# Kernel optimization log

Measured on AMD Instinct MI355X. Metric: run time of the kernel, lower is better.

Reference implementation:

```python
import jax, jax.numpy as jnp
import numpy as np

B, T, D = 16, 8192, 512
NHEAD, NKV = 8, 2
HD = D // NHEAD            # 64
KV_DIM = NKV * HD          # 128
N_REP = NHEAD // NKV       # 4
SCALE = 1.0 / np.sqrt(HD)


def setup_inputs() -> dict:
    key = jax.random.key(0)
    ks = jax.random.split(key, 8)
    w = 0.02
    return {
        "query": jax.random.normal(ks[0], (B, D), dtype=jnp.float32),
        "enc": jax.random.normal(ks[1], (B, T, D), dtype=jnp.float32),
        "Wq": jax.random.normal(ks[2], (D, D), dtype=jnp.float32) * w,
        "Wk": jax.random.normal(ks[3], (D, KV_DIM), dtype=jnp.float32) * w,
        "Wv": jax.random.normal(ks[4], (D, KV_DIM), dtype=jnp.float32) * w,
        "W1": jax.random.normal(ks[5], (2 * D, 4 * D), dtype=jnp.float32) * w,
        "W2": jax.random.normal(ks[6], (4 * D, D), dtype=jnp.float32) * w,
    }


def reference(query, enc, Wq, Wk, Wv, W1, W2):
    # Q projection: single decoder step -> [B, H, HD]
    q = (query @ Wq).reshape(B, NHEAD, HD)
    # K/V projections (GQA): [B, T, NKV, HD] -> [B, NKV, T, HD]
    k = (enc @ Wk).reshape(B, T, NKV, HD).transpose(0, 2, 1, 3)
    v = (enc @ Wv).reshape(B, T, NKV, HD).transpose(0, 2, 1, 3)
    # repeat KV heads to match query heads: [B, H, T, HD]
    k = jnp.repeat(k, N_REP, axis=1)
    v = jnp.repeat(v, N_REP, axis=1)
    # scaled dot-product attention, Tq == 1
    scores = jnp.einsum("bhd,bhtd->bht", q, k) * SCALE        # [B, H, T]
    attn = jax.nn.softmax(scores, axis=-1)
    context = jnp.einsum("bht,bhtd->bhd", attn, v).reshape(B, D)
    # combine context with query through SwiGLU-style MLP (Linear-SiLU-Linear)
    h = jnp.concatenate([context, query], axis=-1)            # [B, 2D]
    out = jax.nn.silu(h @ W1) @ W2                            # [B, D]
    return out
```

## Files before the change

### kernel.cpp

```cpp
#include <hip/hip_runtime.h>
#include <hip/hip_bf16.h>
#include <cstdint>
#include <cstddef>

#define BB 16
#define TT 8192
#define DD 512
#define NHEAD 8
#define NKV 2
#define HD 64
#define KVD 128
#define SCALE 0.125f

#define RB 64
#define NCHUNK (TT / RB)
#define BK 32
#define NSTEP (DD / BK)

typedef __attribute__((ext_vector_type(8))) short bf16x8;
typedef __attribute__((ext_vector_type(4))) float f32x4;

#define WS_Q      0
#define WS_WBT    8192
#define WS_OPART  73728
#define WS_ML     1122304
#define WS_H      1155072
#define WS_APART  1171456
#define WS_M2     1728512

__device__ __forceinline__ ushort f2bf(float f) {
    uint u = __builtin_bit_cast(uint, f);
    u += 0x7fffu + ((u >> 16) & 1u);
    return (ushort)(u >> 16);
}
__device__ __forceinline__ uint cvtpk(float a, float b) {
    uint r;
    asm("v_cvt_pk_bf16_f32 %0, %1, %2" : "=v"(r) : "v"(a), "v"(b));
    return r;
}
__device__ __forceinline__ float bf1(ushort s) {
    return __builtin_bit_cast(float, (uint)s << 16);
}
__device__ __forceinline__ float bflo(uint u) {
    return __builtin_bit_cast(float, u << 16);
}
__device__ __forceinline__ float bfhi(uint u) {
    return __builtin_bit_cast(float, u & 0xffff0000u);
}

__global__ __launch_bounds__(256) void k_prep(const float* __restrict__ Wk,
                                              const float* __restrict__ Wv,
                                              const float* __restrict__ query,
                                              const float* __restrict__ Wq,
                                              ushort* __restrict__ wbt4,
                                              float* __restrict__ wsq) {
    const int t = threadIdx.x;
    if (blockIdx.x < 64) {
        const int G0 = blockIdx.x * 2048 + t * 8;
        const int s = G0 >> 13, r = G0 & 8191;
        const int fid = r >> 9, lane = (r >> 3) & 63;
        const int col = (fid >> 2) * 64 + (fid & 3) * 16 + (lane & 15);
        const int kbase = s * 32 + (lane >> 4) * 8;
        const float* W = (col < KVD) ? (Wk + col) : (Wv + (col - KVD));
#pragma unroll
        for (int e = 0; e < 8; ++e)
            wbt4[G0 + e] = f2bf(W[(size_t)(kbase + e) * KVD]);
    } else {
        __shared__ float qrow[DD];
        const int x = blockIdx.x - 64;
        const int b = x >> 1, half = x & 1;
        qrow[t] = query[b * DD + t];
        qrow[t + 256] = query[b * DD + t + 256];
        __syncthreads();
        const int col = half * 256 + t;
        float a0 = 0.f;
#pragma unroll 8
        for (int d = 0; d < DD; ++d) a0 = fmaf(qrow[d], Wq[(size_t)d * DD + col], a0);
        wsq[b * DD + col] = a0;
    }
}

__global__ __launch_bounds__(256) void k_attn(const float* __restrict__ enc,
                                              const ushort* __restrict__ wbt4,
                                              const float* __restrict__ wsq,
                                              float* __restrict__ o_part,
                                              float* __restrict__ ml) {
    __shared__ __align__(16) char smem[33024];
    __shared__ float sc[NHEAD * RB];
    __shared__ float qs[DD];

    const int tid = threadIdx.x;
    const int chunk = blockIdx.x, b = blockIdx.y;
    const int lane = tid & 63, w = tid >> 6;

    qs[tid] = wsq[b * DD + tid] * SCALE;
    qs[tid + 256] = wsq[b * DD + tid + 256] * SCALE;

    char* const A0 = smem;
    char* const A1 = smem + 4096;
    ushort* const kvl = (ushort*)smem;

    const float* encb = enc + ((size_t)b * TT + (size_t)chunk * RB) * DD;
    const ushort* wfr = wbt4 + ((size_t)w * 256 + lane) * 8;

    const int srow = (tid >> 6) * 16 + (tid & 15);
    const int skb = ((tid >> 4) & 3) * 8;

    f32x4 acc[4][4];
#pragma unroll
    for (int i = 0; i < 4; ++i)
#pragma unroll
        for (int j = 0; j < 4; ++j) acc[i][j] = (f32x4){0.f, 0.f, 0.f, 0.f};

    float4 eA0, eA1, eB0, eB1;
    bf16x8 bfA[4], bfB[4], af[4];

#define LOAD_E(E0, E1, ss)                                                           \
    {                                                                                \
        const float* p_ = encb + (size_t)srow * DD + (ss) * BK + skb;                \
        E0 = *(const float4*)p_;                                                     \
        E1 = *(const float4*)(p_ + 4);                                               \
    }
#define WRITE_A(Abuf, E0, E1)                                                        \
    {                                                                                \
        uint4 u_;                                                                    \
        u_.x = cvtpk(E0.x, E0.y);                                                    \
        u_.y = cvtpk(E0.z, E0.w);                                                    \
        u_.z = cvtpk(E1.x, E1.y);                                                    \
        u_.w = cvtpk(E1.z, E1.w);                                                    \
        *(uint4*)((Abuf) + tid * 16) = u_;                                           \
    }
#define LOAD_B(BF, ss)                                                               \
    {                                                                                \
        _Pragma("unroll") for (int nt = 0; nt < 4; ++nt)                             \
            BF[nt] = *(const bf16x8*)(wfr + (size_t)(ss) * 8192 + nt * 512);         \
    }
#define SYNC()                                                                       \
    {                                                                                \
        __builtin_amdgcn_sched_barrier(0);                                           \
        asm volatile("s_waitcnt lgkmcnt(0)" ::: "memory");                           \
        __builtin_amdgcn_s_barrier();                                                \
    }
#define MFMA_STEP(Ac, BF)                                                            \
    {                                                                                \
        _Pragma("unroll") for (int rt = 0; rt < 4; ++rt)                             \
            af[rt] = *(const bf16x8*)((Ac) + (rt * 64 + lane) * 16);                 \
        _Pragma("unroll") for (int rt = 0; rt < 4; ++rt)                             \
            _Pragma("unroll") for (int nt = 0; nt < 4; ++nt)                         \
                acc[rt][nt] = __builtin_amdgcn_mfma_f32_16x16x32_bf16(               \
                    af[rt], BF[nt], acc[rt][nt], 0, 0, 0);                           \
    }

    LOAD_E(eA0, eA1, 0);
    LOAD_B(bfA, 0);
    LOAD_E(eB0, eB1, 1);
    WRITE_A(A0, eA0, eA1);
    LOAD_E(eA0, eA1, 2);
    SYNC();

#pragma unroll
    for (int s = 0; s < NSTEP; ++s) {
        char* const Ac = (s & 1) ? A1 : A0;
        char* const An = (s & 1) ? A0 : A1;
        if ((s & 1) == 0) {
            if (s + 1 < NSTEP) WRITE_A(An, eB0, eB1);
            if (s + 3 < NSTEP) LOAD_E(eB0, eB1, s + 3);
            if (s + 1 < NSTEP) LOAD_B(bfB, s + 1);
            MFMA_STEP(Ac, bfA);
        } else {
            if (s + 1 < NSTEP) WRITE_A(An, eA0, eA1);
            if (s + 3 < NSTEP) LOAD_E(eA0, eA1, s + 3);
            if (s + 1 < NSTEP) LOAD_B(bfA, s + 1);
            MFMA_STEP(Ac, bfB);
        }
        SYNC();
    }

    const int h0 = w * 2;
    const int kvh = h0 >> 2;

    __syncthreads();
#pragma unroll
    for (int rt = 0; rt < 4; ++rt)
#pragma unroll
        for (int nt = 0; nt < 4; ++nt) {
            const int col = w * 64 + nt * 16 + (lane & 15);
#pragma unroll
            for (int j = 0; j < 4; ++j) {
                const int row = rt * 16 + (lane >> 4) * 4 + j;
                kvl[row * 258 + col] = f2bf(acc[rt][nt][j]);
            }
        }
    __syncthreads();

    {
        const float* qh0 = qs + h0 * HD;
        const float* qh1 = qs + (h0 + 1) * HD;
        const uint* kr = (const uint*)(kvl + lane * 258 + kvh * HD);
        float s0 = 0.f, s1 = 0.f;
#pragma unroll
        for (int d2 = 0; d2 < 32; ++d2) {
            const uint u = kr[d2];
            const float klo = bflo(u), khi = bfhi(u);
            s0 = fmaf(klo, qh0[2 * d2], s0);
            s0 = fmaf(khi, qh0[2 * d2 + 1], s0);
            s1 = fmaf(klo, qh1[2 * d2], s1);
            s1 = fmaf(khi, qh1[2 * d2 + 1], s1);
        }
        sc[h0 * RB + lane] = s0;
        sc[(h0 + 1) * RB + lane] = s1;
    }
    __syncthreads();

    {
        float mx0 = -1e30f, mx1 = -1e30f;
#pragma unroll 8
        for (int r = 0; r < RB; ++r) {
            mx0 = fmaxf(mx0, sc[h0 * RB + r]);
            mx1 = fmaxf(mx1, sc[(h0 + 1) * RB + r]);
        }
        float l0 = 0.f, l1 = 0.f, o0 = 0.f, o1 = 0.f;
        const ushort* vcol = kvl + KVD + kvh * HD + lane;
#pragma unroll 4
        for (int r = 0; r < RB; ++r) {
            const float vv = bf1(vcol[r * 258]);
            const float p0 = __expf(sc[h0 * RB + r] - mx0);
            const float p1 = __expf(sc[(h0 + 1) * RB + r] - mx1);
            l0 += p0; o0 = fmaf(p0, vv, o0);
            l1 += p1; o1 = fmaf(p1, vv, o1);
        }
        const size_t base0 = ((size_t)b * NCHUNK + chunk) * NHEAD + h0;
        o_part[base0 * HD + lane] = o0;
        o_part[(base0 + 1) * HD + lane] = o1;
        if (lane == 0) {
            ml[base0 * 2] = mx0; ml[base0 * 2 + 1] = l0;
            ml[(base0 + 1) * 2] = mx1; ml[(base0 + 1) * 2 + 1] = l1;
        }
    }
#undef LOAD_E
#undef WRITE_A
#undef LOAD_B
#undef SYNC
#undef MFMA_STEP
}

__global__ __launch_bounds__(512) void k_reduce(const float* __restrict__ o_part,
                                                const float* __restrict__ ml,
                                                const float* __restrict__ query,
                                                float* __restrict__ hvec) {
    __shared__ float sEl[NHEAD][NCHUNK];
    const int b = blockIdx.x, t = threadIdx.x;
    const int h = t >> 6, lane = t & 63;

    const size_t ma_i = (((size_t)b * NCHUNK + lane) * NHEAD + h) * 2;
    const size_t mb_i = (((size_t)b * NCHUNK + lane + 64) * NHEAD + h) * 2;
    const float ma = ml[ma_i], la = ml[ma_i + 1];
    const float mb = ml[mb_i], lb = ml[mb_i + 1];
    float M = fmaxf(ma, mb);
#pragma unroll
    for (int off = 32; off >= 1; off >>= 1) M = fmaxf(M, __shfl_xor(M, off));
    const float ea = __expf(ma - M), eb = __expf(mb - M);
    float L = la * ea + lb * eb;
#pragma unroll
    for (int off = 32; off >= 1; off >>= 1) L += __shfl_xor(L, off);
    sEl[h][lane] = ea;
    sEl[h][lane + 64] = eb;
    __syncthreads();

    float O = 0.f;
#pragma unroll 4
    for (int i = 0; i < NCHUNK; ++i) {
        const size_t base = ((size_t)b * NCHUNK + i) * NHEAD + h;
        O = fmaf(o_part[base * HD + lane], sEl[h][i], O);
    }
    hvec[b * 1024 + h * HD + lane] = O / L;
    hvec[b * 1024 + 512 + t] = query[b * DD + t];
}

__global__ __launch_bounds__(256) void k_mlp1(const float* __restrict__ hvec,
                                              const float* __restrict__ W1,
                                              float* __restrict__ apart) {
    const int jb = blockIdx.x, ib = blockIdx.y;
    const int j = jb * 256 + threadIdx.x;
    float acc[BB];
#pragma unroll
    for (int b = 0; b < BB; ++b) acc[b] = 0.f;
    for (int i0 = ib * 64; i0 < ib * 64 + 64; i0 += 4) {
        const float w0 = W1[(size_t)(i0 + 0) * 2048 + j];
        const float w1 = W1[(size_t)(i0 + 1) * 2048 + j];
        const float w2 = W1[(size_t)(i0 + 2) * 2048 + j];
        const float w3 = W1[(size_t)(i0 + 3) * 2048 + j];
#pragma unroll
        for (int b = 0; b < BB; ++b) {
            const float* hb = hvec + b * 1024 + i0;
            acc[b] = fmaf(hb[0], w0, acc[b]);
            acc[b] = fmaf(hb[1], w1, acc[b]);
            acc[b] = fmaf(hb[2], w2, acc[b]);
            acc[b] = fmaf(hb[3], w3, acc[b]);
        }
    }
#pragma unroll
    for (int b = 0; b < BB; ++b)
        apart[((size_t)ib * BB + b) * 2048 + j] = acc[b];
}

__global__ __launch_bounds__(256) void k_mlp2(const float* __restrict__ apart,
                                              const float* __restrict__ W2,
                                              float* __restrict__ m2part) {
    __shared__ float actl[256];
    const int jb = blockIdx.x, b = blockIdx.y, ib = blockIdx.z;
    const int t = threadIdx.x;
    {
        const int jglob = ib * 256 + t;
        float s = 0.f;
#pragma unroll
        for (int p = 0; p < 16; ++p) s += apart[((size_t)p * BB + b) * 2048 + jglob];
        actl[t] = s / (1.f + __expf(-s));
    }
    __syncthreads();
    const int d = jb * 256 + t;
    float acc = 0.f;
    for (int j0 = 0; j0 < 256; j0 += 4) {
        const int jg = ib * 256 + j0;
        acc = fmaf(actl[j0 + 0], W2[(size_t)(jg + 0) * 512 + d], acc);
        acc = fmaf(actl[j0 + 1], W2[(size_t)(jg + 1) * 512 + d], acc);
        acc = fmaf(actl[j0 + 2], W2[(size_t)(jg + 2) * 512 + d], acc);
        acc = fmaf(actl[j0 + 3], W2[(size_t)(jg + 3) * 512 + d], acc);
    }
    m2part[((size_t)ib * BB + b) * 512 + d] = acc;
}

__global__ __launch_bounds__(512) void k_out(const float* __restrict__ m2part,
                                             float* __restrict__ out) {
    const int b = blockIdx.x, t = threadIdx.x;
    float s = 0.f;
#pragma unroll
    for (int ib = 0; ib < 8; ++ib) s += m2part[((size_t)ib * BB + b) * 512 + t];
    out[b * DD + t] = s;
}

extern "C" void kernel_launch(void* const* d_in, const int* in_sizes, int n_in,
                              void* d_out, int out_size, void* d_ws, size_t ws_size,
                              hipStream_t stream) {
    const float* query = (const float*)d_in[0];
    const float* enc   = (const float*)d_in[1];
    const float* Wq    = (const float*)d_in[2];
    const float* Wk    = (const float*)d_in[3];
    const float* Wv    = (const float*)d_in[4];
    const float* W1    = (const float*)d_in[5];
    const float* W2    = (const float*)d_in[6];
    float* ws  = (float*)d_ws;
    float* out = (float*)d_out;
    ushort* wbt4 = (ushort*)(ws + WS_WBT);

    k_prep<<<dim3(96), dim3(256), 0, stream>>>(Wk, Wv, query, Wq, wbt4, ws + WS_Q);
    k_attn<<<dim3(NCHUNK, BB), dim3(256), 0, stream>>>(enc, wbt4, ws + WS_Q,
                                                       ws + WS_OPART, ws + WS_ML);
    k_reduce<<<dim3(BB), dim3(512), 0, stream>>>(ws + WS_OPART, ws + WS_ML, query, ws + WS_H);
    k_mlp1<<<dim3(8, 16), dim3(256), 0, stream>>>(ws + WS_H, W1, ws + WS_APART);
    k_mlp2<<<dim3(2, BB, 8), dim3(256), 0, stream>>>(ws + WS_APART, W2, ws + WS_M2);
    k_out<<<dim3(BB), dim3(512), 0, stream>>>(ws + WS_M2, out);
}
```

Measured before the change: 147.7 us.

## Process two K-steps per barrier in attention GEMM and fuse MLP2 with output reduction

The attention projection loop now handles two BK slices per sync period, using four LDS A buffers and wider enc prefetches. This halves the number of barriers and gives more loads in flight per wait. Separately, k_mlp2 now reduces over all 2048 hidden units inside one block, using four k-slices and an LDS reduction, and writes the output directly. That removes the k_out launch and the partial-sum buffer, but each block recomputes the SiLU activations for all 2048 units.

```diff
diff --git a/kernel.cpp b/kernel.cpp
--- a/kernel.cpp
+++ b/kernel.cpp
@@ -16,6 +16,7 @@
 #define NCHUNK (TT / RB)
 #define BK 32
 #define NSTEP (DD / BK)
+#define NPER (NSTEP / 2)
 
 typedef __attribute__((ext_vector_type(8))) short bf16x8;
 typedef __attribute__((ext_vector_type(4))) float f32x4;
@@ -26,7 +27,6 @@
 #define WS_ML     1122304
 #define WS_H      1155072
 #define WS_APART  1171456
-#define WS_M2     1728512
 
 __device__ __forceinline__ ushort f2bf(float f) {
     uint u = __builtin_bit_cast(uint, f);
@@ -98,6 +98,8 @@
 
     char* const A0 = smem;
     char* const A1 = smem + 4096;
+    char* const A2 = smem + 8192;
+    char* const A3 = smem + 12288;
     ushort* const kvl = (ushort*)smem;
 
     const float* encb = enc + ((size_t)b * TT + (size_t)chunk * RB) * DD;
@@ -112,14 +114,16 @@
 #pragma unroll
         for (int j = 0; j < 4; ++j) acc[i][j] = (f32x4){0.f, 0.f, 0.f, 0.f};
 
-    float4 eA0, eA1, eB0, eB1;
+    float4 e00, e01, e02, e03, e10, e11, e12, e13;
     bf16x8 bfA[4], bfB[4], af[4];
 
-#define LOAD_E(E0, E1, ss)                                                           \
-    {                                                                                \
-        const float* p_ = encb + (size_t)srow * DD + (ss) * BK + skb;                \
-        E0 = *(const float4*)p_;                                                     \
-        E1 = *(const float4*)(p_ + 4);                                               \
+#define LOAD_E2(Ea, Eb, Ec, Ed, s0)                                                  \
+    {                                                                                \
+        const float* p_ = encb + (size_t)srow * DD + (s0) * BK + skb;                \
+        Ea = *(const float4*)p_;                                                     \
+        Eb = *(const float4*)(p_ + 4);                                               \
+        Ec = *(const float4*)(p_ + BK);                                              \
+        Ed = *(const float4*)(p_ + BK + 4);                                          \
     }
 #define WRITE_A(Abuf, E0, E1)                                                        \
     {                                                                                \
@@ -150,31 +154,37 @@
                 acc[rt][nt] = __builtin_amdgcn_mfma_f32_16x16x32_bf16(               \
                     af[rt], BF[nt], acc[rt][nt], 0, 0, 0);                           \
     }
-
-    LOAD_E(eA0, eA1, 0);
+#define DO_PERIOD(p, EW0, EW1, EW2, EW3)                                             \
+    {                                                                                \
+        char* const Ac0_ = ((p) & 1) ? A2 : A0;                                      \
+        char* const Ac1_ = ((p) & 1) ? A3 : A1;                                      \
+        char* const An0_ = ((p) & 1) ? A0 : A2;                                      \
+        char* const An1_ = ((p) & 1) ? A1 : A3;                                      \
+        if ((p) + 1 < NPER) { WRITE_A(An0_, EW0, EW1); WRITE_A(An1_, EW2, EW3); }    \
+        if ((p) < NPER - 3) LOAD_E2(EW0, EW1, EW2, EW3, 2 * (p) + 6);                \
+        LOAD_B(bfB, 2 * (p) + 1);                                                    \
+        MFMA_STEP(Ac0_, bfA);                                                        \
+        if ((p) + 1 < NPER) LOAD_B(bfA, 2 * (p) + 2);                                \
+        MFMA_STEP(Ac1_, bfB);                                                        \
+        SYNC();                                                                      \
+    }
+
+    LOAD_E2(e00, e01, e02, e03, 0);
     LOAD_B(bfA, 0);
-    LOAD_E(eB0, eB1, 1);
-    WRITE_A(A0, eA0, eA1);
-    LOAD_E(eA0, eA1, 2);
+    LOAD_E2(e10, e11, e12, e13, 2);
+    WRITE_A(A0, e00, e01);
+    WRITE_A(A1, e02, e03);
+    LOAD_E2(e00, e01, e02, e03, 4);
     SYNC();
 
-#pragma unroll
-    for (int s = 0; s < NSTEP; ++s) {
-        char* const Ac = (s & 1) ? A1 : A0;
-        char* const An = (s & 1) ? A0 : A1;
-        if ((s & 1) == 0) {
-            if (s + 1 < NSTEP) WRITE_A(An, eB0, eB1);
-            if (s + 3 < NSTEP) LOAD_E(eB0, eB1, s + 3);
-            if (s + 1 < NSTEP) LOAD_B(bfB, s + 1);
-            MFMA_STEP(Ac, bfA);
-        } else {
-            if (s + 1 < NSTEP) WRITE_A(An, eA0, eA1);
-            if (s + 3 < NSTEP) LOAD_E(eA0, eA1, s + 3);
-            if (s + 1 < NSTEP) LOAD_B(bfA, s + 1);
-            MFMA_STEP(Ac, bfB);
-        }
-        SYNC();
-    }
+    DO_PERIOD(0, e10, e11, e12, e13);
+    DO_PERIOD(1, e00, e01, e02, e03);
+    DO_PERIOD(2, e10, e11, e12, e13);
+    DO_PERIOD(3, e00, e01, e02, e03);
+    DO_PERIOD(4, e10, e11, e12, e13);
+    DO_PERIOD(5, e00, e01, e02, e03);
+    DO_PERIOD(6, e10, e11, e12, e13);
+    DO_PERIOD(7, e00, e01, e02, e03);
 
     const int h0 = w * 2;
     const int kvh = h0 >> 2;
@@ -237,11 +247,12 @@
             ml[(base0 + 1) * 2] = mx1; ml[(base0 + 1) * 2 + 1] = l1;
         }
     }
-#undef LOAD_E
+#undef LOAD_E2
 #undef WRITE_A
 #undef LOAD_B
 #undef SYNC
 #undef MFMA_STEP
+#undef DO_PERIOD
 }
 
 __global__ __launch_bounds__(512) void k_reduce(const float* __restrict__ o_part,
@@ -306,37 +317,33 @@
 
 __global__ __launch_bounds__(256) void k_mlp2(const float* __restrict__ apart,
                                               const float* __restrict__ W2,
-                                              float* __restrict__ m2part) {
-    __shared__ float actl[256];
-    const int jb = blockIdx.x, b = blockIdx.y, ib = blockIdx.z;
+                                              float* __restrict__ out) {
+    __shared__ float actl[2048];
+    __shared__ float red[4][64];
+    const int jb = blockIdx.x, b = blockIdx.y;
     const int t = threadIdx.x;
-    {
-        const int jglob = ib * 256 + t;
+#pragma unroll
+    for (int g = 0; g < 8; ++g) {
+        const int j = g * 256 + t;
         float s = 0.f;
 #pragma unroll
-        for (int p = 0; p < 16; ++p) s += apart[((size_t)p * BB + b) * 2048 + jglob];
-        actl[t] = s / (1.f + __expf(-s));
-    }
-    __syncthreads();
-    const int d = jb * 256 + t;
+        for (int p = 0; p < 16; ++p) s += apart[((size_t)p * BB + b) * 2048 + j];
+        actl[j] = s / (1.f + __expf(-s));
+    }
+    __syncthreads();
+    const int d = jb * 64 + (t & 63);
+    const int ks = t >> 6;
     float acc = 0.f;
-    for (int j0 = 0; j0 < 256; j0 += 4) {
-        const int jg = ib * 256 + j0;
-        acc = fmaf(actl[j0 + 0], W2[(size_t)(jg + 0) * 512 + d], acc);
-        acc = fmaf(actl[j0 + 1], W2[(size_t)(jg + 1) * 512 + d], acc);
-        acc = fmaf(actl[j0 + 2], W2[(size_t)(jg + 2) * 512 + d], acc);
-        acc = fmaf(actl[j0 + 3], W2[(size_t)(jg + 3) * 512 + d], acc);
-    }
-    m2part[((size_t)ib * BB + b) * 512 + d] = acc;
-}
-
-__global__ __launch_bounds__(512) void k_out(const float* __restrict__ m2part,
-                                             float* __restrict__ out) {
-    const int b = blockIdx.x, t = threadIdx.x;
-    float s = 0.f;
-#pragma unroll
-    for (int ib = 0; ib < 8; ++ib) s += m2part[((size_t)ib * BB + b) * 512 + t];
-    out[b * DD + t] = s;
+    for (int j0 = ks * 512; j0 < ks * 512 + 512; j0 += 4) {
+        acc = fmaf(actl[j0 + 0], W2[(size_t)(j0 + 0) * 512 + d], acc);
+        acc = fmaf(actl[j0 + 1], W2[(size_t)(j0 + 1) * 512 + d], acc);
+        acc = fmaf(actl[j0 + 2], W2[(size_t)(j0 + 2) * 512 + d], acc);
+        acc = fmaf(actl[j0 + 3], W2[(size_t)(j0 + 3) * 512 + d], acc);
+    }
+    red[ks][t & 63] = acc;
+    __syncthreads();
+    if (t < 64)
+        out[b * DD + jb * 64 + t] = red[0][t] + red[1][t] + red[2][t] + red[3][t];
 }
 
 extern "C" void kernel_launch(void* const* d_in, const int* in_sizes, int n_in,
@@ -358,6 +365,5 @@
                                                        ws + WS_OPART, ws + WS_ML);
     k_reduce<<<dim3(BB), dim3(512), 0, stream>>>(ws + WS_OPART, ws + WS_ML, query, ws + WS_H);
     k_mlp1<<<dim3(8, 16), dim3(256), 0, stream>>>(ws + WS_H, W1, ws + WS_APART);
-    k_mlp2<<<dim3(2, BB, 8), dim3(256), 0, stream>>>(ws + WS_APART, W2, ws + WS_M2);
-    k_out<<<dim3(BB), dim3(512), 0, stream>>>(ws + WS_M2, out);
-}
+    k_mlp2<<<dim3(8, BB), dim3(256), 0, stream>>>(ws + WS_APART, W2, out);
+}
```

Result: slower. 154.8 us (+4.8%).
